# Performance work log

Hardware: AMD Instinct MI355X
Metric: run time of the kernel (lower is better)

The kernel has to match this reference:

```python
import jax, jax.numpy as jnp
import numpy as np

N = 100000
E = 1600000
D = 64
K = 2


def setup_inputs() -> dict:
    key = jax.random.key(0)
    k1, k2, k3 = jax.random.split(key, 3)
    x = jax.random.normal(k1, (N, D), dtype=jnp.float32)
    edge_index = jax.random.randint(k2, (2, E), 0, N, dtype=jnp.int64)
    # glorot-initialized linear: [(K+1)*D, D_out]
    fan_in, fan_out = (K + 1) * D, D
    limit = float(np.sqrt(6.0 / (fan_in + fan_out)))
    W = jax.random.uniform(k3, (fan_in, fan_out), dtype=jnp.float32, minval=-limit, maxval=limit)
    b = jnp.zeros((fan_out,), dtype=jnp.float32)
    return {"x": x, "edge_index": edge_index, "W": W, "b": b}


def reference(x, edge_index, W, b):
    n = x.shape[0]
    src = edge_index[0]
    dst = edge_index[1]
    # gcn_norm with add_self_loops=True, edge_weight=None -> ones
    loop = jnp.arange(n, dtype=src.dtype)
    src = jnp.concatenate([src, loop])
    dst = jnp.concatenate([dst, loop])
    w = jnp.ones(src.shape[0], dtype=x.dtype)
    deg = jax.ops.segment_sum(w, dst, num_segments=n)
    dinv = jnp.where(deg > 0, jax.lax.rsqrt(deg), jnp.zeros_like(deg))
    wn = dinv[src] * w * dinv[dst]  # D^-1/2 A_hat D^-1/2 edge weights
    xs = [x]
    h = x
    for _ in range(K):
        # spmm: out[i] = sum_{(j->i)} w_ji * h[j]
        h = jax.ops.segment_sum(wn[:, None] * h[src], dst, num_segments=n)
        xs.append(h)
    feats = jnp.concatenate(xs, axis=-1)  # [N, (K+1)*D]
    return feats @ W + b
```

## Files before the change

kernel.cpp:

```cpp
#include <hip/hip_runtime.h>

#define D_FEAT 64
#define CHUNK 4096
#define NBMAX 512
#define BNODES 256

typedef __attribute__((ext_vector_type(8))) short bf16x8;
typedef __attribute__((ext_vector_type(4))) float f32x4;

static __device__ inline short f2bf(float f) {
    unsigned u = __float_as_uint(f);
    u += 0x7fffu + ((u >> 16) & 1u);
    return (short)(u >> 16);
}

static __device__ inline void acc8(uint4 u, float* a) {
    a[0] += __uint_as_float(u.x << 16);
    a[1] += __uint_as_float(u.x & 0xffff0000u);
    a[2] += __uint_as_float(u.y << 16);
    a[3] += __uint_as_float(u.y & 0xffff0000u);
    a[4] += __uint_as_float(u.z << 16);
    a[5] += __uint_as_float(u.z & 0xffff0000u);
    a[6] += __uint_as_float(u.w << 16);
    a[7] += __uint_as_float(u.w & 0xffff0000u);
}

static __device__ inline uint4 pack8(const float* a, float s) {
    uint4 r;
    r.x = (unsigned)(unsigned short)f2bf(a[0] * s) | ((unsigned)(unsigned short)f2bf(a[1] * s) << 16);
    r.y = (unsigned)(unsigned short)f2bf(a[2] * s) | ((unsigned)(unsigned short)f2bf(a[3] * s) << 16);
    r.z = (unsigned)(unsigned short)f2bf(a[4] * s) | ((unsigned)(unsigned short)f2bf(a[5] * s) << 16);
    r.w = (unsigned)(unsigned short)f2bf(a[6] * s) | ((unsigned)(unsigned short)f2bf(a[7] * s) << 16);
    return r;
}


__global__ __launch_bounds__(256) void hist_kernel(const int* __restrict__ dst,
                                                   int* __restrict__ hist,
                                                   int e, int nb) {
    __shared__ int hs[NBMAX];
    int tid = threadIdx.x;
    for (int i = tid; i < nb; i += 256) hs[i] = 0;
    __syncthreads();
    int base = blockIdx.x * CHUNK;
    int end = min(base + CHUNK, e);
    for (int i = base + tid; i < end; i += 256)
        atomicAdd(&hs[dst[i] >> 8], 1);
    __syncthreads();
    for (int i = tid; i < nb; i += 256)
        hist[(size_t)blockIdx.x * nb + i] = hs[i];
}


__global__ __launch_bounds__(512) void colscan_kernel(int* __restrict__ hist,
                                                      int* __restrict__ totals,
                                                      int nc, int nb) {
    __shared__ int s[512];
    int k = blockIdx.x;
    int t = threadIdx.x;
    int v = (t < nc) ? hist[(size_t)t * nb + k] : 0;
    s[t] = v;
    __syncthreads();
    for (int off = 1; off < 512; off <<= 1) {
        int u = (t >= off) ? s[t - off] : 0;
        __syncthreads();
        s[t] += u;
        __syncthreads();
    }
    if (t < nc) hist[(size_t)t * nb + k] = s[t] - v;
    if (t == nc - 1) totals[k] = s[t];
}


__global__ __launch_bounds__(512) void base_kernel(const int* __restrict__ totals,
                                                   int* __restrict__ bbase,
                                                   int* __restrict__ rp,
                                                   int nb, int n, int e) {
    __shared__ int s[512];
    int t = threadIdx.x;
    int v = (t < nb) ? totals[t] : 0;
    s[t] = v;
    __syncthreads();
    for (int off = 1; off < 512; off <<= 1) {
        int u = (t >= off) ? s[t - off] : 0;
        __syncthreads();
        s[t] += u;
        __syncthreads();
    }
    if (t < nb) bbase[t] = s[t] - v;
    if (t == 0) {
        bbase[nb] = e;
        rp[n] = e;
    }
}


__global__ __launch_bounds__(256) void scatter_kernel(const int* __restrict__ src,
                                                      const int* __restrict__ dst,
                                                      const int* __restrict__ pref,
                                                      const int* __restrict__ bbase,
                                                      int2* __restrict__ pairs,
                                                      int e, int nb) {
    __shared__ int cur[NBMAX];
    int tid = threadIdx.x;
    int b = blockIdx.x;
    for (int i = tid; i < nb; i += 256)
        cur[i] = bbase[i] + pref[(size_t)b * nb + i];
    __syncthreads();
    int base = b * CHUNK;
    int end = min(base + CHUNK, e);
    for (int i = base + tid; i < end; i += 256) {
        int d = dst[i];
        int pos = atomicAdd(&cur[d >> 8], 1);
        pairs[pos] = make_int2(d, src[i]);
    }
}


__global__ __launch_bounds__(256) void csr_kernel(const int2* __restrict__ pairs,
                                                  const int* __restrict__ bbase,
                                                  int* __restrict__ rp,
                                                  float* __restrict__ dinv,
                                                  int* __restrict__ col, int n) {
    __shared__ int cnt[BNODES];
    __shared__ int s[BNODES];
    __shared__ int cur[BNODES];
    int tid = threadIdx.x;
    int k = blockIdx.x;
    int node0 = k * BNODES;
    int e0 = bbase[k];
    int e1 = bbase[k + 1];
    cnt[tid] = 0;
    __syncthreads();
    for (int i = e0 + tid; i < e1; i += 256)
        atomicAdd(&cnt[pairs[i].x - node0], 1);
    __syncthreads();
    int v = cnt[tid];
    s[tid] = v;
    __syncthreads();
    for (int off = 1; off < 256; off <<= 1) {
        int u = (tid >= off) ? s[tid - off] : 0;
        __syncthreads();
        s[tid] += u;
        __syncthreads();
    }
    int excl = s[tid] - v;
    cur[tid] = e0 + excl;
    int node = node0 + tid;
    if (node < n) {
        rp[node] = e0 + excl;
        dinv[node] = rsqrtf(1.0f + (float)v);
    }
    __syncthreads();
    for (int i = e0 + tid; i < e1; i += 256) {
        int2 p = pairs[i];
        int pos = atomicAdd(&cur[p.x - node0], 1);
        col[pos] = p.y;
    }
}


__global__ __launch_bounds__(256) void convert_kernel(const float* __restrict__ x,
                                                      const float* __restrict__ dinv,
                                                      uint4* __restrict__ xb,
                                                      uint4* __restrict__ xs, int n) {
    int t = blockIdx.x * 256 + threadIdx.x;
    int node = t >> 3;
    int j = t & 7;
    if (node >= n) return;
    const float4* x4 = (const float4*)x;
    float4 a0 = x4[(size_t)node * 16 + j * 2];
    float4 a1 = x4[(size_t)node * 16 + j * 2 + 1];
    float di = dinv[node];
    float a[8] = {a0.x, a0.y, a0.z, a0.w, a1.x, a1.y, a1.z, a1.w};
    size_t o = (size_t)node * 8 + j;
    xb[o] = pack8(a, 1.0f);
    xs[o] = pack8(a, di);
}


__global__ __launch_bounds__(256) void spmm_hop1_kernel(const int* __restrict__ rp,
                                                        const int* __restrict__ col,
                                                        const float* __restrict__ dinv,
                                                        const uint4* __restrict__ xs,
                                                        uint4* __restrict__ h1b,
                                                        uint4* __restrict__ g1b, int n) {
    int t = blockIdx.x * 256 + threadIdx.x;
    int node = t >> 3;
    int j = t & 7;
    if (node >= n) return;
    int e0 = rp[node];
    int e1 = rp[node + 1];
    float di = dinv[node];
    float a[8] = {0, 0, 0, 0, 0, 0, 0, 0};
    float c[8] = {0, 0, 0, 0, 0, 0, 0, 0};
    acc8(xs[(size_t)node * 8 + j], a);
    int e = e0;
    for (; e + 1 < e1; e += 2) {
        int s0 = col[e];
        int s1 = col[e + 1];
        uint4 u0 = xs[(size_t)s0 * 8 + j];
        uint4 u1 = xs[(size_t)s1 * 8 + j];
        acc8(u0, a);
        acc8(u1, c);
    }
    if (e < e1) acc8(xs[(size_t)col[e] * 8 + j], a);
#pragma unroll
    for (int i = 0; i < 8; ++i) a[i] += c[i];
    size_t o = (size_t)node * 8 + j;
    h1b[o] = pack8(a, di);
    g1b[o] = pack8(a, di * di);
}


__global__ __launch_bounds__(256) void spmm_hop2_kernel(const int* __restrict__ rp,
                                                        const int* __restrict__ col,
                                                        const float* __restrict__ dinv,
                                                        const uint4* __restrict__ g1b,
                                                        uint4* __restrict__ h2b, int n) {
    int t = blockIdx.x * 256 + threadIdx.x;
    int node = t >> 3;
    int j = t & 7;
    if (node >= n) return;
    int e0 = rp[node];
    int e1 = rp[node + 1];
    float di = dinv[node];
    float a[8] = {0, 0, 0, 0, 0, 0, 0, 0};
    float c[8] = {0, 0, 0, 0, 0, 0, 0, 0};
    acc8(g1b[(size_t)node * 8 + j], a);
    int e = e0;
    for (; e + 1 < e1; e += 2) {
        int s0 = col[e];
        int s1 = col[e + 1];
        uint4 u0 = g1b[(size_t)s0 * 8 + j];
        uint4 u1 = g1b[(size_t)s1 * 8 + j];
        acc8(u0, a);
        acc8(u1, c);
    }
    if (e < e1) acc8(g1b[(size_t)col[e] * 8 + j], a);
#pragma unroll
    for (int i = 0; i < 8; ++i) a[i] += c[i];
    h2b[(size_t)node * 8 + j] = pack8(a, di);
}


#define WT_LD 200

__global__ __launch_bounds__(256) void gemm_mfma_kernel(const unsigned short* __restrict__ xb,
                                                        const unsigned short* __restrict__ h1b,
                                                        const unsigned short* __restrict__ h2b,
                                                        const float* __restrict__ W,
                                                        const float* __restrict__ b,
                                                        float* __restrict__ out, int n) {
    __shared__ short sWt[64 * WT_LD];
    int tid = threadIdx.x;

    for (int i = tid; i < 192 * 64; i += 256) {
        int k = i >> 6;
        int c = i & 63;
        sWt[c * WT_LD + k] = f2bf(W[i]);
    }
    __syncthreads();

    int w = tid >> 6;
    int l = tid & 63;
    int lr = l & 15;
    int lk = l >> 4;
    int rbase = blockIdx.x * 64 + w * 16;

    int node = rbase + lr;
    int node_ld = node < n ? node : (n - 1);

    f32x4 acc[4] = {{0.f, 0.f, 0.f, 0.f}, {0.f, 0.f, 0.f, 0.f},
                    {0.f, 0.f, 0.f, 0.f}, {0.f, 0.f, 0.f, 0.f}};

    const unsigned short* srcs[3] = {xb, h1b, h2b};
#pragma unroll
    for (int kt = 0; kt < 6; ++kt) {
        const unsigned short* sp = srcs[kt >> 1];
        int kb = (kt & 1) * 32 + lk * 8;
        bf16x8 af = *(const bf16x8*)(sp + (size_t)node_ld * D_FEAT + kb);
        int kg = kt * 32 + lk * 8;
#pragma unroll
        for (int nt = 0; nt < 4; ++nt) {
            int c = nt * 16 + lr;
            bf16x8 bf = *(const bf16x8*)&sWt[c * WT_LD + kg];
            acc[nt] = __builtin_amdgcn_mfma_f32_16x16x32_bf16(af, bf, acc[nt], 0, 0, 0);
        }
    }

#pragma unroll
    for (int nt = 0; nt < 4; ++nt) {
        int c = nt * 16 + lr;
        float bias = b[c];
#pragma unroll
        for (int i = 0; i < 4; ++i) {
            int row = rbase + lk * 4 + i;
            if (row < n) out[(size_t)row * D_FEAT + c] = acc[nt][i] + bias;
        }
    }
}


static inline size_t align256(size_t x) { return (x + 255) & ~(size_t)255; }

extern "C" void kernel_launch(void* const* d_in, const int* in_sizes, int n_in,
                              void* d_out, int out_size, void* d_ws, size_t ws_size,
                              hipStream_t stream) {
    const float* x  = (const float*)d_in[0];
    const int*   ei = (const int*)d_in[1];
    const float* W  = (const float*)d_in[2];
    const float* b  = (const float*)d_in[3];
    float* out = (float*)d_out;

    int N = in_sizes[0] / D_FEAT;
    int E = in_sizes[1] / 2;
    const int* src = ei;
    const int* dst = ei + E;

    int NB = (N + BNODES - 1) / BNODES;
    int NC = (E + CHUNK - 1) / CHUNK;

    char* base = (char*)d_ws;
    size_t off = 0;
    int* rp      = (int*)(base + off);   off = align256(off + ((size_t)N + 1) * 4);
    float* dinv  = (float*)(base + off); off = align256(off + (size_t)N * 4);
    int* totals  = (int*)(base + off);   off = align256(off + (size_t)NBMAX * 4);
    int* bbase   = (int*)(base + off);   off = align256(off + (size_t)(NBMAX + 1) * 4);
    int* col     = (int*)(base + off);   off = align256(off + (size_t)E * 4);
    uint4* xb    = (uint4*)(base + off); off = align256(off + (size_t)N * D_FEAT * 2);
    uint4* xs    = (uint4*)(base + off); off = align256(off + (size_t)N * D_FEAT * 2);
    uint4* h1b   = (uint4*)(base + off); off = align256(off + (size_t)N * D_FEAT * 2);
    uint4* g1b   = (uint4*)(base + off); off = align256(off + (size_t)N * D_FEAT * 2);
    uint4* h2b   = (uint4*)(base + off); off = align256(off + (size_t)N * D_FEAT * 2);
    int2* pairs  = (int2*)(base + off);
    int* hist    = (int*)((char*)pairs + align256((size_t)E * 8));

    const int BS = 256;
    int gN8 = (int)(((long long)N * 8 + BS - 1) / BS);
    int gGemm = (N + 63) / 64;

    hist_kernel<<<NC, BS, 0, stream>>>(dst, hist, E, NB);
    colscan_kernel<<<NB, 512, 0, stream>>>(hist, totals, NC, NB);
    base_kernel<<<1, 512, 0, stream>>>(totals, bbase, rp, NB, N, E);
    scatter_kernel<<<NC, BS, 0, stream>>>(src, dst, hist, bbase, pairs, E, NB);
    csr_kernel<<<NB, BS, 0, stream>>>(pairs, bbase, rp, dinv, col, N);
    convert_kernel<<<gN8, BS, 0, stream>>>(x, dinv, xb, xs, N);
    spmm_hop1_kernel<<<gN8, BS, 0, stream>>>(rp, col, dinv, xs, h1b, g1b, N);
    spmm_hop2_kernel<<<gN8, BS, 0, stream>>>(rp, col, dinv, g1b, h2b, N);
    gemm_mfma_kernel<<<gGemm, BS, 0, stream>>>((const unsigned short*)xb,
                                               (const unsigned short*)h1b,
                                               (const unsigned short*)h2b,
                                               W, b, out, N);
}
```

Before: 217.3 us.

## Pack scatter pairs to 32 bits, drop h1 buffer, unroll SpMM gathers by four

```diff
diff --git a/kernel.cpp b/kernel.cpp
--- a/kernel.cpp
+++ b/kernel.cpp
@@ -99,7 +99,7 @@
                                                       const int* __restrict__ dst,
                                                       const int* __restrict__ pref,
                                                       const int* __restrict__ bbase,
-                                                      int2* __restrict__ pairs,
+                                                      unsigned* __restrict__ pairs,
                                                       int e, int nb) {
     __shared__ int cur[NBMAX];
     int tid = threadIdx.x;
@@ -112,12 +112,12 @@
     for (int i = base + tid; i < end; i += 256) {
         int d = dst[i];
         int pos = atomicAdd(&cur[d >> 8], 1);
-        pairs[pos] = make_int2(d, src[i]);
-    }
-}
-
-
-__global__ __launch_bounds__(256) void csr_kernel(const int2* __restrict__ pairs,
+        pairs[pos] = ((unsigned)(d & 255) << 24) | (unsigned)src[i];
+    }
+}
+
+
+__global__ __launch_bounds__(256) void csr_kernel(const unsigned* __restrict__ pairs,
                                                   const int* __restrict__ bbase,
                                                   int* __restrict__ rp,
                                                   float* __restrict__ dinv,
@@ -133,7 +133,7 @@
     cnt[tid] = 0;
     __syncthreads();
     for (int i = e0 + tid; i < e1; i += 256)
-        atomicAdd(&cnt[pairs[i].x - node0], 1);
+        atomicAdd(&cnt[pairs[i] >> 24], 1);
     __syncthreads();
     int v = cnt[tid];
     s[tid] = v;
@@ -153,9 +153,9 @@
     }
     __syncthreads();
     for (int i = e0 + tid; i < e1; i += 256) {
-        int2 p = pairs[i];
-        int pos = atomicAdd(&cur[p.x - node0], 1);
-        col[pos] = p.y;
+        unsigned p = pairs[i];
+        int pos = atomicAdd(&cur[p >> 24], 1);
+        col[pos] = (int)(p & 0xFFFFFFu);
     }
 }
 
@@ -183,7 +183,6 @@
                                                         const int* __restrict__ col,
                                                         const float* __restrict__ dinv,
                                                         const uint4* __restrict__ xs,
-                                                        uint4* __restrict__ h1b,
                                                         uint4* __restrict__ g1b, int n) {
     int t = blockIdx.x * 256 + threadIdx.x;
     int node = t >> 3;
@@ -196,20 +195,24 @@
     float c[8] = {0, 0, 0, 0, 0, 0, 0, 0};
     acc8(xs[(size_t)node * 8 + j], a);
     int e = e0;
-    for (; e + 1 < e1; e += 2) {
+    for (; e + 3 < e1; e += 4) {
         int s0 = col[e];
         int s1 = col[e + 1];
+        int s2 = col[e + 2];
+        int s3 = col[e + 3];
         uint4 u0 = xs[(size_t)s0 * 8 + j];
         uint4 u1 = xs[(size_t)s1 * 8 + j];
+        uint4 u2 = xs[(size_t)s2 * 8 + j];
+        uint4 u3 = xs[(size_t)s3 * 8 + j];
         acc8(u0, a);
         acc8(u1, c);
-    }
-    if (e < e1) acc8(xs[(size_t)col[e] * 8 + j], a);
+        acc8(u2, a);
+        acc8(u3, c);
+    }
+    for (; e < e1; ++e) acc8(xs[(size_t)col[e] * 8 + j], a);
 #pragma unroll
     for (int i = 0; i < 8; ++i) a[i] += c[i];
-    size_t o = (size_t)node * 8 + j;
-    h1b[o] = pack8(a, di);
-    g1b[o] = pack8(a, di * di);
+    g1b[(size_t)node * 8 + j] = pack8(a, di * di);
 }
 
 
@@ -229,15 +232,21 @@
     float c[8] = {0, 0, 0, 0, 0, 0, 0, 0};
     acc8(g1b[(size_t)node * 8 + j], a);
     int e = e0;
-    for (; e + 1 < e1; e += 2) {
+    for (; e + 3 < e1; e += 4) {
         int s0 = col[e];
         int s1 = col[e + 1];
+        int s2 = col[e + 2];
+        int s3 = col[e + 3];
         uint4 u0 = g1b[(size_t)s0 * 8 + j];
         uint4 u1 = g1b[(size_t)s1 * 8 + j];
+        uint4 u2 = g1b[(size_t)s2 * 8 + j];
+        uint4 u3 = g1b[(size_t)s3 * 8 + j];
         acc8(u0, a);
         acc8(u1, c);
-    }
-    if (e < e1) acc8(g1b[(size_t)col[e] * 8 + j], a);
+        acc8(u2, a);
+        acc8(u3, c);
+    }
+    for (; e < e1; ++e) acc8(g1b[(size_t)col[e] * 8 + j], a);
 #pragma unroll
     for (int i = 0; i < 8; ++i) a[i] += c[i];
     h2b[(size_t)node * 8 + j] = pack8(a, di);
@@ -247,8 +256,9 @@
 #define WT_LD 200
 
 __global__ __launch_bounds__(256) void gemm_mfma_kernel(const unsigned short* __restrict__ xb,
-                                                        const unsigned short* __restrict__ h1b,
+                                                        const unsigned short* __restrict__ g1b,
                                                         const unsigned short* __restrict__ h2b,
+                                                        const float* __restrict__ dinv,
                                                         const float* __restrict__ W,
                                                         const float* __restrict__ b,
                                                         float* __restrict__ out, int n) {
@@ -271,10 +281,12 @@
     int node = rbase + lr;
     int node_ld = node < n ? node : (n - 1);
 
-    f32x4 acc[4] = {{0.f, 0.f, 0.f, 0.f}, {0.f, 0.f, 0.f, 0.f},
-                    {0.f, 0.f, 0.f, 0.f}, {0.f, 0.f, 0.f, 0.f}};
-
-    const unsigned short* srcs[3] = {xb, h1b, h2b};
+    f32x4 accA[4] = {{0.f, 0.f, 0.f, 0.f}, {0.f, 0.f, 0.f, 0.f},
+                     {0.f, 0.f, 0.f, 0.f}, {0.f, 0.f, 0.f, 0.f}};
+    f32x4 accB[4] = {{0.f, 0.f, 0.f, 0.f}, {0.f, 0.f, 0.f, 0.f},
+                     {0.f, 0.f, 0.f, 0.f}, {0.f, 0.f, 0.f, 0.f}};
+
+    const unsigned short* srcs[3] = {xb, g1b, h2b};
 #pragma unroll
     for (int kt = 0; kt < 6; ++kt) {
         const unsigned short* sp = srcs[kt >> 1];
@@ -285,8 +297,18 @@
         for (int nt = 0; nt < 4; ++nt) {
             int c = nt * 16 + lr;
             bf16x8 bf = *(const bf16x8*)&sWt[c * WT_LD + kg];
-            acc[nt] = __builtin_amdgcn_mfma_f32_16x16x32_bf16(af, bf, acc[nt], 0, 0, 0);
+            if ((kt >> 1) == 1)
+                accB[nt] = __builtin_amdgcn_mfma_f32_16x16x32_bf16(af, bf, accB[nt], 0, 0, 0);
+            else
+                accA[nt] = __builtin_amdgcn_mfma_f32_16x16x32_bf16(af, bf, accA[nt], 0, 0, 0);
         }
+    }
+
+    float sd[4];
+#pragma unroll
+    for (int i = 0; i < 4; ++i) {
+        int row = rbase + lk * 4 + i;
+        sd[i] = (row < n) ? (1.0f / dinv[row]) : 0.0f;
     }
 
 #pragma unroll
@@ -296,7 +318,8 @@
 #pragma unroll
         for (int i = 0; i < 4; ++i) {
             int row = rbase + lk * 4 + i;
-            if (row < n) out[(size_t)row * D_FEAT + c] = acc[nt][i] + bias;
+            if (row < n)
+                out[(size_t)row * D_FEAT + c] = accA[nt][i] + sd[i] * accB[nt][i] + bias;
         }
     }
 }
@@ -330,11 +353,10 @@
     int* col     = (int*)(base + off);   off = align256(off + (size_t)E * 4);
     uint4* xb    = (uint4*)(base + off); off = align256(off + (size_t)N * D_FEAT * 2);
     uint4* xs    = (uint4*)(base + off); off = align256(off + (size_t)N * D_FEAT * 2);
-    uint4* h1b   = (uint4*)(base + off); off = align256(off + (size_t)N * D_FEAT * 2);
     uint4* g1b   = (uint4*)(base + off); off = align256(off + (size_t)N * D_FEAT * 2);
     uint4* h2b   = (uint4*)(base + off); off = align256(off + (size_t)N * D_FEAT * 2);
-    int2* pairs  = (int2*)(base + off);
-    int* hist    = (int*)((char*)pairs + align256((size_t)E * 8));
+    unsigned* pairs = (unsigned*)(base + off);
+    int* hist    = (int*)((char*)pairs + align256((size_t)E * 4));
 
     const int BS = 256;
     int gN8 = (int)(((long long)N * 8 + BS - 1) / BS);
@@ -346,10 +368,10 @@
     scatter_kernel<<<NC, BS, 0, stream>>>(src, dst, hist, bbase, pairs, E, NB);
     csr_kernel<<<NB, BS, 0, stream>>>(pairs, bbase, rp, dinv, col, N);
     convert_kernel<<<gN8, BS, 0, stream>>>(x, dinv, xb, xs, N);
-    spmm_hop1_kernel<<<gN8, BS, 0, stream>>>(rp, col, dinv, xs, h1b, g1b, N);
+    spmm_hop1_kernel<<<gN8, BS, 0, stream>>>(rp, col, dinv, xs, g1b, N);
     spmm_hop2_kernel<<<gN8, BS, 0, stream>>>(rp, col, dinv, g1b, h2b, N);
     gemm_mfma_kernel<<<gGemm, BS, 0, stream>>>((const unsigned short*)xb,
-                                               (const unsigned short*)h1b,
+                                               (const unsigned short*)g1b,
                                                (const unsigned short*)h2b,
-                                               W, b, out, N);
-}
+                                               dinv, W, b, out, N);
+}
```

Result: no change. 217.3 us (-0.0%).
